# Performance work log

Measured on AMD Instinct MI355X. Metric: run time of the kernel, lower is better.

Reference implementation:

```python
import jax, jax.numpy as jnp
import numpy as np

B, L, D = 4, 896, 2048
HQ, HKV, HD = 32, 8, 64
GROUP = HQ // HKV          # 4
TOKENS_PER_FRAME = 7
ROPE_BASE = 10000.0


def setup_inputs() -> dict:
    key = jax.random.key(0)
    ks = jax.random.split(key, 5)
    s = 0.02
    return {
        "x": jax.random.normal(ks[0], (B, L, D), jnp.float32),
        "wq": jax.random.normal(ks[1], (D, D), jnp.float32) * s,
        "wk": jax.random.normal(ks[2], (D, HKV * HD), jnp.float32) * s,
        "wv": jax.random.normal(ks[3], (D, HKV * HD), jnp.float32) * s,
        "wo": jax.random.normal(ks[4], (D, D), jnp.float32) * s,
        "pos_ids": jnp.arange(L, dtype=jnp.int32),
    }


def _apply_rotary(t, cos, sin):
    # t: [B, L, H, HD]; rotate all HD dims, interleaved pairs.
    Bt, Lt, Ht, Hd = t.shape
    tp = t.reshape(Bt, Lt, Ht, Hd // 2, 2)
    x1, x2 = tp[..., 0], tp[..., 1]
    c = cos[None, :, None, :]   # [1, L, 1, HD/2]
    s = sin[None, :, None, :]
    y1 = x1 * c - x2 * s
    y2 = x1 * s + x2 * c
    return jnp.stack([y1, y2], axis=-1).reshape(Bt, Lt, Ht, Hd)


def reference(x, wq, wk, wv, wo, pos_ids):
    Bx, Lx, Dx = x.shape
    q = (x @ wq).reshape(Bx, Lx, HQ, HD)
    k = (x @ wk).reshape(Bx, Lx, HKV, HD)
    v = (x @ wv).reshape(Bx, Lx, HKV, HD)

    # RoPE (rot_dim = head_dim), scale = 1.0
    half = HD // 2
    inv_freq = 1.0 / (ROPE_BASE ** (jnp.arange(half, dtype=jnp.float32) / half))
    freqs = pos_ids.astype(jnp.float32)[:, None] * inv_freq[None, :]  # [L, HD/2]
    cos, sin = jnp.cos(freqs), jnp.sin(freqs)
    q = _apply_rotary(q, cos, sin)
    k = _apply_rotary(k, cos, sin)

    # GQA: expand kv heads to q heads (kv_head = q_head // GROUP)
    k = jnp.repeat(k, GROUP, axis=2)   # [B, L, HQ, HD]
    v = jnp.repeat(v, GROUP, axis=2)

    scale = 1.0 / jnp.sqrt(jnp.float32(HD))
    scores = jnp.einsum('blhd,bmhd->bhlm', q, k) * scale  # [B, HQ, L, L]

    # frame-block causal mask: allow key frame <= query frame
    pos = jnp.arange(Lx)
    fid = pos // TOKENS_PER_FRAME
    allow = fid[None, :] <= fid[:, None]                  # [L, L]
    neg = jnp.finfo(scores.dtype).min
    scores = jnp.where(allow[None, None], scores, neg)

    probs = jax.nn.softmax(scores, axis=-1)
    out = jnp.einsum('bhlm,bmhd->blhd', probs, v).reshape(Bx, Lx, Dx)
    return out @ wo
```

## Files before the change

### kernel.cpp

```cpp
#include <hip/hip_runtime.h>
#include <hip/hip_bf16.h>
#include <cstdint>

typedef __bf16 bf16;
typedef __bf16 bf16x8 __attribute__((ext_vector_type(8)));
typedef float floatx4 __attribute__((ext_vector_type(4)));

#define B_   4
#define L_   896
#define D_   2048
#define HQ_  32
#define HKV_ 8
#define HD_  64
#define NQKV 3072
#define M_   3584

__device__ inline void gl_lds16(const bf16* g, bf16* l) {
    __builtin_amdgcn_global_load_lds(
        (const __attribute__((address_space(1))) void*)g,
        (__attribute__((address_space(3))) void*)l, 16, 0, 0);
}

__device__ inline void barrier_() {
    asm volatile("" ::: "memory");
    __builtin_amdgcn_s_barrier();
    asm volatile("" ::: "memory");
}

__global__ __launch_bounds__(256) void convert_to_bf16(const float* __restrict__ in,
                                                       bf16* __restrict__ out) {
    long q = (long)blockIdx.x * 256 + threadIdx.x;
    float4 v = ((const float4*)in)[q];
    union { bf16 b[4]; ushort4 u; } w;
    w.b[0] = (bf16)v.x; w.b[1] = (bf16)v.y; w.b[2] = (bf16)v.z; w.b[3] = (bf16)v.w;
    ((ushort4*)out)[q] = w.u;
}

__global__ __launch_bounds__(256) void rope_cs_kernel(const int* __restrict__ pos_ids,
                                                      float2* __restrict__ cs) {
    int idx = blockIdx.x * 256 + threadIdx.x;
    if (idx >= L_ * 32) return;
    int l = idx >> 5, i = idx & 31;
    float p = (float)pos_ids[l];
    float inv = exp2f(-(float)i * (13.287712379549449f / 32.0f));
    float a = p * inv;
    cs[idx] = make_float2(cosf(a), sinf(a));
}

__global__ __launch_bounds__(256) void rope_apply(bf16* __restrict__ QKV,
                                                  const float2* __restrict__ cs) {
    int idx = blockIdx.x * 256 + threadIdx.x;
    int m = idx / 320, g = idx - m * 320;
    int l = m % L_;
    int hp = (g * 4) & 31;
    const float2* ct = &cs[l * 32 + hp];
    bf16* p = QKV + (long)m * NQKV + g * 8;
    bf16x8 v = *(bf16x8*)p;
    bf16x8 w;
#pragma unroll
    for (int i = 0; i < 4; i++) {
        float2 csv = ct[i];
        float x1 = (float)v[2 * i], x2 = (float)v[2 * i + 1];
        w[2 * i]     = (bf16)(x1 * csv.x - x2 * csv.y);
        w[2 * i + 1] = (bf16)(x1 * csv.y + x2 * csv.x);
    }
    *(bf16x8*)p = w;
}

__global__ __launch_bounds__(256) void transpose_cvt(
    const float* __restrict__ in, ushort* __restrict__ out, int C, int R) {
    __shared__ ushort t[64][72];
    int tid = threadIdx.x;
    int tr = tid >> 4, tc = (tid & 15) << 2;
    long r0 = (long)blockIdx.y << 6, c0 = (long)blockIdx.x << 6;
#pragma unroll
    for (int i = 0; i < 4; ++i) {
        float4 v = *(const float4*)&in[(r0 + tr + i * 16) * C + c0 + tc];
        union { bf16 b[4]; ushort4 u; } w;
        w.b[0] = (bf16)v.x; w.b[1] = (bf16)v.y; w.b[2] = (bf16)v.z; w.b[3] = (bf16)v.w;
        *(ushort4*)&t[tr + i * 16][tc] = w.u;
    }
    __syncthreads();
#pragma unroll
    for (int i = 0; i < 4; ++i) {
        ushort4 w;
        w.x = t[tc + 0][tr + i * 16];
        w.y = t[tc + 1][tr + i * 16];
        w.z = t[tc + 2][tr + i * 16];
        w.w = t[tc + 3][tr + i * 16];
        *(ushort4*)&out[(c0 + tr + i * 16) * R + r0 + tc] = w;
    }
}

__global__ __launch_bounds__(256) void transpose_u16(
    const ushort* __restrict__ in, ushort* __restrict__ out,
    int ld_in, int ld_out, long is1, long is2, long os1, long os2) {
    __shared__ ushort t[64][72];
    int z = blockIdx.z;
    const ushort* ip = in + (long)(z >> 3) * is1 + (long)(z & 7) * is2;
    ushort* op = out + (long)(z >> 3) * os1 + (long)(z & 7) * os2;
    int tid = threadIdx.x;
    int tr = tid >> 4, tc = (tid & 15) << 2;
    long r0 = (long)blockIdx.y << 6, c0 = (long)blockIdx.x << 6;
#pragma unroll
    for (int i = 0; i < 4; ++i) {
        ushort4 v = *(const ushort4*)&ip[(r0 + tr + i * 16) * ld_in + c0 + tc];
        *(ushort4*)&t[tr + i * 16][tc] = v;
    }
    __syncthreads();
#pragma unroll
    for (int i = 0; i < 4; ++i) {
        ushort4 w;
        w.x = t[tc + 0][tr + i * 16];
        w.y = t[tc + 1][tr + i * 16];
        w.z = t[tc + 2][tr + i * 16];
        w.w = t[tc + 3][tr + i * 16];
        *(ushort4*)&op[(c0 + tr + i * 16) * ld_out + r0 + tc] = w;
    }
}

template <int JF, int OUTF32>
__global__ __launch_bounds__(512, 2) void gemm224(
    const bf16* __restrict__ A, const bf16* __restrict__ Bt, void* __restrict__ C,
    int Ntot, int Ktot) {
    __shared__ bf16 ldsA[2][224 * 64];
    __shared__ bf16 ldsB[2][JF * 64 * 64];
    const int tid = threadIdx.x;
    const int lane = tid & 63;
    const int quad = lane >> 4, l16 = lane & 15;
    const int w = tid >> 6;
    const int wr = w >> 2, wc = w & 3;

    const int gx = gridDim.x;
    const int nwg = gx * gridDim.y;
    int orig = blockIdx.y * gx + blockIdx.x;
    int q8 = nwg >> 3, r8 = nwg & 7;
    int xcd = orig & 7, lid = orig >> 3;
    int wg = (xcd < r8 ? xcd * (q8 + 1) : r8 * (q8 + 1) + (xcd - r8) * q8) + lid;
    const long m0 = (long)(wg / gx) * 224;
    const long n0 = (long)(wg % gx) * (JF * 64);

    const long rowK = Ktot;
    const int srow = tid >> 3;
    const int scol = ((tid & 7) ^ (srow & 7)) << 3;
    const bf16* baseA = A  + (m0 + srow) * rowK + scol;
    const bf16* baseB = Bt + (n0 + srow) * rowK + scol;
    bf16* const dA = (bf16*)ldsA + tid * 8;
    bf16* const dB = (bf16*)ldsB + tid * 8;

    const int m7 = l16 & 7;
    const int col0 = ((0 + quad) ^ m7) << 3;
    const int col1 = ((4 + quad) ^ m7) << 3;
    const int abase = wr * 112 + l16;
    const int bbase = wc * (JF * 16) + l16;

    floatx4 acc[7][JF];
#pragma unroll
    for (int i = 0; i < 7; ++i)
#pragma unroll
        for (int j = 0; j < JF; ++j)
#pragma unroll
            for (int r = 0; r < 4; ++r) acc[i][j][r] = 0.f;

    bf16x8 af0[4][2], af1[3][2], bq[JF][2];

    const int T = Ktot >> 6;

    {
        gl_lds16(baseA,              dA);
        gl_lds16(baseA + 64 * rowK,  dA + 4096);
        gl_lds16(baseA + 128 * rowK, dA + 8192);
        if (tid < 256) gl_lds16(baseA + 192 * rowK, dA + 12288);
#pragma unroll
        for (int r = 0; r < JF; ++r) gl_lds16(baseB + r * 64 * rowK, dB + r * 4096);
#pragma unroll
        for (int r = 0; r < JF; ++r) gl_lds16(baseB + 64 + r * 64 * rowK,
                                              dB + JF * 4096 + r * 4096);
    }
    if (JF == 3) asm volatile("s_waitcnt vmcnt(3)" ::: "memory");
    else         asm volatile("s_waitcnt vmcnt(2)" ::: "memory");
    barrier_();

    for (int t = 0; t < T; ++t) {
        const int cur = t & 1, nxt = cur ^ 1;
        const bf16* pa = &ldsA[cur][0];
        const bf16* pb = &ldsB[cur][0];
        const long koff  = (long)(t + 1) * 64;
        const long koff2 = (long)(t + 2) * 64;

#pragma unroll
        for (int i = 0; i < 4; ++i) {
            const bf16* rp = &pa[(abase + i * 16) * 64];
            af0[i][0] = *(const bf16x8*)&rp[col0];
            af0[i][1] = *(const bf16x8*)&rp[col1];
        }
#pragma unroll
        for (int j = 0; j < JF; ++j) {
            const bf16* rp = &pb[(bbase + j * 16) * 64];
            bq[j][0] = *(const bf16x8*)&rp[col0];
            bq[j][1] = *(const bf16x8*)&rp[col1];
        }
        if (t + 1 < T) {
            const bf16* g = baseA + koff;
            bf16* l = dA + nxt * (224 * 64);
            gl_lds16(g,              l);
            gl_lds16(g + 64 * rowK,  l + 4096);
            gl_lds16(g + 128 * rowK, l + 8192);
            if (tid < 256) gl_lds16(g + 192 * rowK, l + 12288);
        }
        barrier_();
        asm volatile("s_waitcnt lgkmcnt(0)" ::: "memory");
        __builtin_amdgcn_sched_barrier(0);
        __builtin_amdgcn_s_setprio(1);
#pragma unroll
        for (int i = 0; i < 4; ++i)
#pragma unroll
            for (int j = 0; j < JF; ++j) {
                floatx4 c = acc[i][j];
                c = __builtin_amdgcn_mfma_f32_16x16x32_bf16(af0[i][0], bq[j][0], c, 0, 0, 0);
                c = __builtin_amdgcn_mfma_f32_16x16x32_bf16(af0[i][1], bq[j][1], c, 0, 0, 0);
                acc[i][j] = c;
            }
        __builtin_amdgcn_s_setprio(0);
        barrier_();

#pragma unroll
        for (int i = 0; i < 3; ++i) {
            const bf16* rp = &pa[(abase + (4 + i) * 16) * 64];
            af1[i][0] = *(const bf16x8*)&rp[col0];
            af1[i][1] = *(const bf16x8*)&rp[col1];
        }
        if (t + 2 < T) {
            const bf16* g = baseB + koff2;
            bf16* l = dB + cur * (JF * 64 * 64);
#pragma unroll
            for (int r = 0; r < JF; ++r) gl_lds16(g + r * 64 * rowK, l + r * 4096);
        }
        barrier_();
        asm volatile("s_waitcnt lgkmcnt(0)" ::: "memory");
        __builtin_amdgcn_sched_barrier(0);
        __builtin_amdgcn_s_setprio(1);
#pragma unroll
        for (int i = 0; i < 3; ++i)
#pragma unroll
            for (int j = 0; j < JF; ++j) {
                floatx4 c = acc[4 + i][j];
                c = __builtin_amdgcn_mfma_f32_16x16x32_bf16(af1[i][0], bq[j][0], c, 0, 0, 0);
                c = __builtin_amdgcn_mfma_f32_16x16x32_bf16(af1[i][1], bq[j][1], c, 0, 0, 0);
                acc[4 + i][j] = c;
            }
        __builtin_amdgcn_s_setprio(0);
        if (t + 2 < T) {
            if (JF == 3) asm volatile("s_waitcnt vmcnt(3)" ::: "memory");
            else         asm volatile("s_waitcnt vmcnt(2)" ::: "memory");
        } else {
            asm volatile("s_waitcnt vmcnt(0)" ::: "memory");
        }
        barrier_();
    }

#pragma unroll
    for (int i = 0; i < 7; ++i)
#pragma unroll
        for (int j = 0; j < JF; ++j)
#pragma unroll
            for (int r = 0; r < 4; ++r) {
                long m = m0 + wr * 112 + i * 16 + quad * 4 + r;
                long n = n0 + wc * (JF * 16) + j * 16 + l16;
                if (OUTF32) ((float*)C)[m * Ntot + n] = acc[i][j][r];
                else        ((bf16*)C)[m * Ntot + n] = (bf16)acc[i][j][r];
            }
}

__global__ __launch_bounds__(256) void attn_kernel(
    const bf16* __restrict__ QKV,
    const bf16* __restrict__ Vt,
    bf16* __restrict__ AO) {
    __shared__ bf16 Ks[64 * 64];
    __shared__ bf16 Vs[64 * 64];
    __shared__ bf16 Ps[4][32 * 76];
    const int tid  = threadIdx.x;
    const int wid  = tid >> 6, lane = tid & 63;
    const int quad = lane >> 4, c = lane & 15;
    const int b = blockIdx.z;
    const int kvh = blockIdx.y >> 1, hp = blockIdx.y & 1;
    const int hq = kvh * 4 + hp * 2 + (wid >> 1);
    const int sub = wid & 1;
    const int xpair = blockIdx.x;
    bf16* ps = &Ps[wid][0];

    const bf16* Kb = QKV + ((long)(b * L_)) * NQKV + D_ + kvh * HD_;
    const bf16* Vb = Vt + ((long)(b * HKV_ + kvh)) * (HD_ * L_);

    const int srow = tid >> 3, schunk = (tid & 7) << 3;
    const int sslot = ((tid & 7) ^ (srow & 7)) << 3;
    const bf16* kp0 = &Kb[(long)srow * NQKV + schunk];
    const bf16* kp1 = &Kb[(long)(32 + srow) * NQKV + schunk];
    const bf16* vp0 = &Vb[(long)srow * L_ + schunk];
    const bf16* vp1 = &Vb[(long)(srow + 32) * L_ + schunk];

    const int m7 = c & 7;
    const int col0 = ((0 + quad) ^ m7) << 3;
    const int col1 = ((4 + quad) ^ m7) << 3;

    const floatx4 fzero = {0.f, 0.f, 0.f, 0.f};
    const float C1 = 0.18033688011112042f;

#pragma unroll 1
    for (int pass = 0; pass < 2; ++pass) {
        const int x = pass == 0 ? xpair : 13 - xpair;
        const int q0b = x * 64;
        const bf16* Qb = QKV + ((long)(b * L_ + q0b + sub * 32)) * NQKV + hq * HD_;

        bf16x8 qf[2][2];
#pragma unroll
        for (int a = 0; a < 2; a++) {
            qf[a][0] = *(const bf16x8*)&Qb[(long)(a * 16 + c) * NQKV + quad * 8];
            qf[a][1] = *(const bf16x8*)&Qb[(long)(a * 16 + c) * NQKV + 32 + quad * 8];
        }

        float lsum[2][4];
        floatx4 o[2][4];
#pragma unroll
        for (int a = 0; a < 2; a++)
#pragma unroll
            for (int r = 0; r < 4; r++) lsum[a][r] = 0.f;
#pragma unroll
        for (int a = 0; a < 2; a++)
#pragma unroll
            for (int nt = 0; nt < 4; nt++)
#pragma unroll
                for (int r = 0; r < 4; r++) o[a][nt][r] = 0.f;

        int fe[2][4];
#pragma unroll
        for (int a = 0; a < 2; a++)
#pragma unroll
            for (int r = 0; r < 4; r++) {
                int l = q0b + sub * 32 + a * 16 + quad * 4 + r;
                fe[a][r] = (l / 7 + 1) * 7;
            }
        const int femin = (q0b / 7 + 1) * 7;
        const int kend  = ((q0b + 63) / 7 + 1) * 7;

        bf16x8 kg0 = *(const bf16x8*)&kp0[0];
        bf16x8 kg1 = *(const bf16x8*)&kp1[0];
        bf16x8 vg0 = *(const bf16x8*)&vp0[0];
        bf16x8 vg1 = *(const bf16x8*)&vp1[0];

        for (int k0 = 0; k0 < kend; k0 += 64) {
            __syncthreads();
            *(bf16x8*)&Ks[srow * 64 + sslot]        = kg0;
            *(bf16x8*)&Ks[(srow + 32) * 64 + sslot] = kg1;
            *(bf16x8*)&Vs[srow * 64 + sslot]        = vg0;
            *(bf16x8*)&Vs[(srow + 32) * 64 + sslot] = vg1;
            __syncthreads();

            const int kn = k0 + 64;
            if (kn < kend) {
                kg0 = *(const bf16x8*)&kp0[(long)kn * NQKV];
                kg1 = *(const bf16x8*)&kp1[(long)kn * NQKV];
                vg0 = *(const bf16x8*)&vp0[kn];
                vg1 = *(const bf16x8*)&vp1[kn];
            }

            bf16x8 kf[4][2];
#pragma unroll
            for (int n = 0; n < 4; n++) {
                const bf16* rp = &Ks[(n * 16 + c) * 64];
                kf[n][0] = *(bf16x8*)&rp[col0];
                kf[n][1] = *(bf16x8*)&rp[col1];
            }
            const int masked = (k0 + 64 > femin);
#pragma unroll
            for (int a = 0; a < 2; a++) {
                floatx4 s[4];
#pragma unroll
                for (int n = 0; n < 4; n++) {
                    s[n] = __builtin_amdgcn_mfma_f32_16x16x32_bf16(qf[a][0], kf[n][0], fzero, 0, 0, 0);
                    s[n] = __builtin_amdgcn_mfma_f32_16x16x32_bf16(qf[a][1], kf[n][1], s[n], 0, 0, 0);
                }
                if (masked) {
#pragma unroll
                    for (int n = 0; n < 4; n++) {
                        const int key = k0 + n * 16 + c;
#pragma unroll
                        for (int r = 0; r < 4; r++) {
                            float e = exp2f(s[n][r] * C1);
                            e = (key < fe[a][r]) ? e : 0.f;
                            lsum[a][r] += e;
                            ps[(a * 16 + quad * 4 + r) * 76 + n * 16 + c] = (bf16)e;
                        }
                    }
                } else {
#pragma unroll
                    for (int n = 0; n < 4; n++) {
#pragma unroll
                        for (int r = 0; r < 4; r++) {
                            float e = exp2f(s[n][r] * C1);
                            lsum[a][r] += e;
                            ps[(a * 16 + quad * 4 + r) * 76 + n * 16 + c] = (bf16)e;
                        }
                    }
                }
            }
            bf16x8 vf[4][2];
#pragma unroll
            for (int nt = 0; nt < 4; nt++) {
                const bf16* rp = &Vs[(nt * 16 + c) * 64];
                vf[nt][0] = *(bf16x8*)&rp[col0];
                vf[nt][1] = *(bf16x8*)&rp[col1];
            }
#pragma unroll
            for (int a = 0; a < 2; a++) {
                bf16x8 pf0 = *(bf16x8*)&ps[(a * 16 + c) * 76 + quad * 8];
                bf16x8 pf1 = *(bf16x8*)&ps[(a * 16 + c) * 76 + 32 + quad * 8];
#pragma unroll
                for (int nt = 0; nt < 4; nt++) {
                    o[a][nt] = __builtin_amdgcn_mfma_f32_16x16x32_bf16(pf0, vf[nt][0], o[a][nt], 0, 0, 0);
                    o[a][nt] = __builtin_amdgcn_mfma_f32_16x16x32_bf16(pf1, vf[nt][1], o[a][nt], 0, 0, 0);
                }
            }
        }
#pragma unroll
        for (int a = 0; a < 2; a++)
#pragma unroll
            for (int r = 0; r < 4; r++) {
#pragma unroll
                for (int off = 1; off < 16; off <<= 1)
                    lsum[a][r] += __shfl_xor(lsum[a][r], off);
            }
#pragma unroll
        for (int a = 0; a < 2; a++)
#pragma unroll
            for (int nt = 0; nt < 4; nt++)
#pragma unroll
                for (int r = 0; r < 4; r++) {
                    int l = q0b + sub * 32 + a * 16 + quad * 4 + r;
                    AO[((long)(b * L_ + l)) * D_ + hq * HD_ + nt * 16 + c] =
                        (bf16)(o[a][nt][r] / lsum[a][r]);
                }
    }
}

extern "C" void kernel_launch(void* const* d_in, const int* in_sizes, int n_in,
                              void* d_out, int out_size, void* d_ws, size_t ws_size,
                              hipStream_t stream) {
    (void)in_sizes; (void)n_in; (void)out_size; (void)ws_size;
    const float* x  = (const float*)d_in[0];
    const float* wq = (const float*)d_in[1];
    const float* wk = (const float*)d_in[2];
    const float* wv = (const float*)d_in[3];
    const float* wo = (const float*)d_in[4];
    const int* pos  = (const int*)d_in[5];

    bf16* ws    = (bf16*)d_ws;
    bf16* xb    = ws;
    bf16* wqkvT = ws + 7340032L;
    bf16* woT   = ws + 13631488L;
    bf16* QKV   = ws + 17825792L;
    bf16* Vt    = ws + 28835840L;
    bf16* AO    = xb;
    float2* cs  = (float2*)(ws + 30670848L);

    convert_to_bf16<<<dim3(7168), 256, 0, stream>>>(x, xb);
    rope_cs_kernel<<<dim3(112), dim3(256), 0, stream>>>(pos, cs);

    transpose_cvt<<<dim3(32, 32), 256, 0, stream>>>(wq, (ushort*)wqkvT, 2048, 2048);
    transpose_cvt<<<dim3(8, 32), 256, 0, stream>>>(wk, (ushort*)(wqkvT + 4194304L), 512, 2048);
    transpose_cvt<<<dim3(8, 32), 256, 0, stream>>>(wv, (ushort*)(wqkvT + 5242880L), 512, 2048);
    transpose_cvt<<<dim3(32, 32), 256, 0, stream>>>(wo, (ushort*)woT, 2048, 2048);

    gemm224<3, 0><<<dim3(16, 16), 512, 0, stream>>>(xb, wqkvT, QKV, NQKV, D_);

    rope_apply<<<dim3(4480), 256, 0, stream>>>(QKV, cs);

    transpose_u16<<<dim3(1, 14, 32), 256, 0, stream>>>(
        (const ushort*)(QKV + 2560), (ushort*)Vt, 3072, 896,
        896L * 3072, 64, 8L * 57344, 57344);

    attn_kernel<<<dim3(7, 16, 4), 256, 0, stream>>>(QKV, Vt, AO);

    gemm224<2, 1><<<dim3(16, 16), 512, 0, stream>>>(AO, woT, d_out, D_, D_);
}
```

Baseline: 269.6 us.

## Fuse prep kernels into one launch and double attention KV tile to 128

Merges the x conversion, the four weight transpose-converts and the RoPE cos/sin table into a single prep kernel, so six launches become one and their work shares one grid. The attention kernel now stages 128 keys per iteration, with a wider swizzled V tile, and processes two 64-key halves between barriers. This halves the number of barrier/staging rounds and prefetch phases. The cost is more shared memory and more prefetch registers per block, which may lower occupancy.

```diff
diff --git a/kernel.cpp b/kernel.cpp
--- a/kernel.cpp
+++ b/kernel.cpp
@@ -25,26 +25,6 @@
     asm volatile("" ::: "memory");
     __builtin_amdgcn_s_barrier();
     asm volatile("" ::: "memory");
-}
-
-__global__ __launch_bounds__(256) void convert_to_bf16(const float* __restrict__ in,
-                                                       bf16* __restrict__ out) {
-    long q = (long)blockIdx.x * 256 + threadIdx.x;
-    float4 v = ((const float4*)in)[q];
-    union { bf16 b[4]; ushort4 u; } w;
-    w.b[0] = (bf16)v.x; w.b[1] = (bf16)v.y; w.b[2] = (bf16)v.z; w.b[3] = (bf16)v.w;
-    ((ushort4*)out)[q] = w.u;
-}
-
-__global__ __launch_bounds__(256) void rope_cs_kernel(const int* __restrict__ pos_ids,
-                                                      float2* __restrict__ cs) {
-    int idx = blockIdx.x * 256 + threadIdx.x;
-    if (idx >= L_ * 32) return;
-    int l = idx >> 5, i = idx & 31;
-    float p = (float)pos_ids[l];
-    float inv = exp2f(-(float)i * (13.287712379549449f / 32.0f));
-    float a = p * inv;
-    cs[idx] = make_float2(cosf(a), sinf(a));
 }
 
 __global__ __launch_bounds__(256) void rope_apply(bf16* __restrict__ QKV,
@@ -67,12 +47,11 @@
     *(bf16x8*)p = w;
 }
 
-__global__ __launch_bounds__(256) void transpose_cvt(
-    const float* __restrict__ in, ushort* __restrict__ out, int C, int R) {
-    __shared__ ushort t[64][72];
-    int tid = threadIdx.x;
+__device__ inline void tr_cvt_body(const float* __restrict__ in,
+                                   ushort* __restrict__ out, int C, int R,
+                                   int bx, int by, int tid, ushort (*t)[72]) {
     int tr = tid >> 4, tc = (tid & 15) << 2;
-    long r0 = (long)blockIdx.y << 6, c0 = (long)blockIdx.x << 6;
+    long r0 = (long)by << 6, c0 = (long)bx << 6;
 #pragma unroll
     for (int i = 0; i < 4; ++i) {
         float4 v = *(const float4*)&in[(r0 + tr + i * 16) * C + c0 + tc];
@@ -89,6 +68,44 @@
         w.z = t[tc + 2][tr + i * 16];
         w.w = t[tc + 3][tr + i * 16];
         *(ushort4*)&out[(c0 + tr + i * 16) * R + r0 + tc] = w;
+    }
+}
+
+__global__ __launch_bounds__(256) void prep_kernel(
+    const float* __restrict__ x, const float* __restrict__ wq,
+    const float* __restrict__ wk, const float* __restrict__ wv,
+    const float* __restrict__ wo, const int* __restrict__ pos_ids,
+    bf16* __restrict__ xb, bf16* __restrict__ wqkvT, bf16* __restrict__ woT,
+    float2* __restrict__ cs) {
+    __shared__ ushort t[64][72];
+    const int d = blockIdx.x, tid = threadIdx.x;
+    if (d < 7168) {
+        long q = (long)d * 256 + tid;
+        float4 v = ((const float4*)x)[q];
+        union { bf16 b[4]; ushort4 u; } w;
+        w.b[0] = (bf16)v.x; w.b[1] = (bf16)v.y; w.b[2] = (bf16)v.z; w.b[3] = (bf16)v.w;
+        ((ushort4*)xb)[q] = w.u;
+    } else if (d < 8192) {
+        int e = d - 7168;
+        tr_cvt_body(wq, (ushort*)wqkvT, 2048, 2048, e & 31, e >> 5, tid, t);
+    } else if (d < 9216) {
+        int e = d - 8192;
+        tr_cvt_body(wo, (ushort*)woT, 2048, 2048, e & 31, e >> 5, tid, t);
+    } else if (d < 9472) {
+        int e = d - 9216;
+        tr_cvt_body(wk, (ushort*)(wqkvT + 4194304L), 512, 2048, e & 7, e >> 3, tid, t);
+    } else if (d < 9728) {
+        int e = d - 9472;
+        tr_cvt_body(wv, (ushort*)(wqkvT + 5242880L), 512, 2048, e & 7, e >> 3, tid, t);
+    } else {
+        int idx = (d - 9728) * 256 + tid;
+        if (idx < L_ * 32) {
+            int l = idx >> 5, i = idx & 31;
+            float p = (float)pos_ids[l];
+            float inv = exp2f(-(float)i * (13.287712379549449f / 32.0f));
+            float a = p * inv;
+            cs[idx] = make_float2(cosf(a), sinf(a));
+        }
     }
 }
 
@@ -276,8 +293,8 @@
     const bf16* __restrict__ QKV,
     const bf16* __restrict__ Vt,
     bf16* __restrict__ AO) {
-    __shared__ bf16 Ks[64 * 64];
-    __shared__ bf16 Vs[64 * 64];
+    __shared__ bf16 Ks[128 * 64];
+    __shared__ bf16 Vs[64 * 128];
     __shared__ bf16 Ps[4][32 * 76];
     const int tid  = threadIdx.x;
     const int wid  = tid >> 6, lane = tid & 63;
@@ -292,16 +309,14 @@
     const bf16* Kb = QKV + ((long)(b * L_)) * NQKV + D_ + kvh * HD_;
     const bf16* Vb = Vt + ((long)(b * HKV_ + kvh)) * (HD_ * L_);
 
-    const int srow = tid >> 3, schunk = (tid & 7) << 3;
-    const int sslot = ((tid & 7) ^ (srow & 7)) << 3;
-    const bf16* kp0 = &Kb[(long)srow * NQKV + schunk];
-    const bf16* kp1 = &Kb[(long)(32 + srow) * NQKV + schunk];
-    const bf16* vp0 = &Vb[(long)srow * L_ + schunk];
-    const bf16* vp1 = &Vb[(long)(srow + 32) * L_ + schunk];
+    const int srowK = tid >> 3, schunkK = (tid & 7) << 3;
+    const int sslotK = ((tid & 7) ^ (srowK & 7)) << 3;
+    const int srowV = tid >> 4, schunkV = (tid & 15) << 3;
+    const int sslotV = ((tid & 15) ^ (srowV & 15)) << 3;
 
     const int m7 = c & 7;
-    const int col0 = ((0 + quad) ^ m7) << 3;
-    const int col1 = ((4 + quad) ^ m7) << 3;
+    const int colK0 = ((0 + quad) ^ m7) << 3;
+    const int colK1 = ((4 + quad) ^ m7) << 3;
 
     const floatx4 fzero = {0.f, 0.f, 0.f, 0.f};
     const float C1 = 0.18033688011112042f;
@@ -343,82 +358,95 @@
         const int femin = (q0b / 7 + 1) * 7;
         const int kend  = ((q0b + 63) / 7 + 1) * 7;
 
-        bf16x8 kg0 = *(const bf16x8*)&kp0[0];
-        bf16x8 kg1 = *(const bf16x8*)&kp1[0];
-        bf16x8 vg0 = *(const bf16x8*)&vp0[0];
-        bf16x8 vg1 = *(const bf16x8*)&vp1[0];
-
-        for (int k0 = 0; k0 < kend; k0 += 64) {
+        bf16x8 kgr[4], vgr[4];
+#pragma unroll
+        for (int j = 0; j < 4; j++)
+            kgr[j] = *(const bf16x8*)&Kb[(long)(srowK + 32 * j) * NQKV + schunkK];
+#pragma unroll
+        for (int j = 0; j < 4; j++)
+            vgr[j] = *(const bf16x8*)&Vb[(long)(srowV + 16 * j) * L_ + schunkV];
+
+        for (int k0 = 0; k0 < kend; k0 += 128) {
             __syncthreads();
-            *(bf16x8*)&Ks[srow * 64 + sslot]        = kg0;
-            *(bf16x8*)&Ks[(srow + 32) * 64 + sslot] = kg1;
-            *(bf16x8*)&Vs[srow * 64 + sslot]        = vg0;
-            *(bf16x8*)&Vs[(srow + 32) * 64 + sslot] = vg1;
+#pragma unroll
+            for (int j = 0; j < 4; j++)
+                *(bf16x8*)&Ks[(srowK + 32 * j) * 64 + sslotK] = kgr[j];
+#pragma unroll
+            for (int j = 0; j < 4; j++)
+                *(bf16x8*)&Vs[(srowV + 16 * j) * 128 + sslotV] = vgr[j];
             __syncthreads();
 
-            const int kn = k0 + 64;
+            const int kn = k0 + 128;
             if (kn < kend) {
-                kg0 = *(const bf16x8*)&kp0[(long)kn * NQKV];
-                kg1 = *(const bf16x8*)&kp1[(long)kn * NQKV];
-                vg0 = *(const bf16x8*)&vp0[kn];
-                vg1 = *(const bf16x8*)&vp1[kn];
-            }
-
-            bf16x8 kf[4][2];
-#pragma unroll
-            for (int n = 0; n < 4; n++) {
-                const bf16* rp = &Ks[(n * 16 + c) * 64];
-                kf[n][0] = *(bf16x8*)&rp[col0];
-                kf[n][1] = *(bf16x8*)&rp[col1];
-            }
-            const int masked = (k0 + 64 > femin);
-#pragma unroll
-            for (int a = 0; a < 2; a++) {
-                floatx4 s[4];
+#pragma unroll
+                for (int j = 0; j < 4; j++)
+                    kgr[j] = *(const bf16x8*)&Kb[(long)(kn + srowK + 32 * j) * NQKV + schunkK];
+#pragma unroll
+                for (int j = 0; j < 4; j++)
+                    vgr[j] = *(const bf16x8*)&Vb[(long)(srowV + 16 * j) * L_ + kn + schunkV];
+            }
+
+#pragma unroll
+            for (int h = 0; h < 2; h++) {
+                const int kb = k0 + 64 * h;
+                if (kb >= kend) break;
+
+                bf16x8 kf[4][2];
 #pragma unroll
                 for (int n = 0; n < 4; n++) {
-                    s[n] = __builtin_amdgcn_mfma_f32_16x16x32_bf16(qf[a][0], kf[n][0], fzero, 0, 0, 0);
-                    s[n] = __builtin_amdgcn_mfma_f32_16x16x32_bf16(qf[a][1], kf[n][1], s[n], 0, 0, 0);
+                    const bf16* rp = &Ks[(64 * h + n * 16 + c) * 64];
+                    kf[n][0] = *(bf16x8*)&rp[colK0];
+                    kf[n][1] = *(bf16x8*)&rp[colK1];
                 }
-                if (masked) {
+                const int masked = (kb + 64 > femin);
+#pragma unroll
+                for (int a = 0; a < 2; a++) {
+                    floatx4 s[4];
 #pragma unroll
                     for (int n = 0; n < 4; n++) {
-                        const int key = k0 + n * 16 + c;
-#pragma unroll
-                        for (int r = 0; r < 4; r++) {
-                            float e = exp2f(s[n][r] * C1);
-                            e = (key < fe[a][r]) ? e : 0.f;
-                            lsum[a][r] += e;
-                            ps[(a * 16 + quad * 4 + r) * 76 + n * 16 + c] = (bf16)e;
+                        s[n] = __builtin_amdgcn_mfma_f32_16x16x32_bf16(qf[a][0], kf[n][0], fzero, 0, 0, 0);
+                        s[n] = __builtin_amdgcn_mfma_f32_16x16x32_bf16(qf[a][1], kf[n][1], s[n], 0, 0, 0);
+                    }
+                    if (masked) {
+#pragma unroll
+                        for (int n = 0; n < 4; n++) {
+                            const int key = kb + n * 16 + c;
+#pragma unroll
+                            for (int r = 0; r < 4; r++) {
+                                float e = exp2f(s[n][r] * C1);
+                                e = (key < fe[a][r]) ? e : 0.f;
+                                lsum[a][r] += e;
+                                ps[(a * 16 + quad * 4 + r) * 76 + n * 16 + c] = (bf16)e;
+                            }
                         }
-                    }
-                } else {
-#pragma unroll
-                    for (int n = 0; n < 4; n++) {
-#pragma unroll
-                        for (int r = 0; r < 4; r++) {
-                            float e = exp2f(s[n][r] * C1);
-                            lsum[a][r] += e;
-                            ps[(a * 16 + quad * 4 + r) * 76 + n * 16 + c] = (bf16)e;
+                    } else {
+#pragma unroll
+                        for (int n = 0; n < 4; n++) {
+#pragma unroll
+                            for (int r = 0; r < 4; r++) {
+                                float e = exp2f(s[n][r] * C1);
+                                lsum[a][r] += e;
+                                ps[(a * 16 + quad * 4 + r) * 76 + n * 16 + c] = (bf16)e;
+                            }
                         }
                     }
                 }
-            }
-            bf16x8 vf[4][2];
-#pragma unroll
-            for (int nt = 0; nt < 4; nt++) {
-                const bf16* rp = &Vs[(nt * 16 + c) * 64];
-                vf[nt][0] = *(bf16x8*)&rp[col0];
-                vf[nt][1] = *(bf16x8*)&rp[col1];
-            }
-#pragma unroll
-            for (int a = 0; a < 2; a++) {
-                bf16x8 pf0 = *(bf16x8*)&ps[(a * 16 + c) * 76 + quad * 8];
-                bf16x8 pf1 = *(bf16x8*)&ps[(a * 16 + c) * 76 + 32 + quad * 8];
+                bf16x8 vf[4][2];
 #pragma unroll
                 for (int nt = 0; nt < 4; nt++) {
-                    o[a][nt] = __builtin_amdgcn_mfma_f32_16x16x32_bf16(pf0, vf[nt][0], o[a][nt], 0, 0, 0);
-                    o[a][nt] = __builtin_amdgcn_mfma_f32_16x16x32_bf16(pf1, vf[nt][1], o[a][nt], 0, 0, 0);
+                    const bf16* rp = &Vs[(nt * 16 + c) * 128];
+                    vf[nt][0] = *(bf16x8*)&rp[(((8 * h + 0 + quad) ^ c) << 3)];
+                    vf[nt][1] = *(bf16x8*)&rp[(((8 * h + 4 + quad) ^ c) << 3)];
+                }
+#pragma unroll
+                for (int a = 0; a < 2; a++) {
+                    bf16x8 pf0 = *(bf16x8*)&ps[(a * 16 + c) * 76 + quad * 8];
+                    bf16x8 pf1 = *(bf16x8*)&ps[(a * 16 + c) * 76 + 32 + quad * 8];
+#pragma unroll
+                    for (int nt = 0; nt < 4; nt++) {
+                        o[a][nt] = __builtin_amdgcn_mfma_f32_16x16x32_bf16(pf0, vf[nt][0], o[a][nt], 0, 0, 0);
+                        o[a][nt] = __builtin_amdgcn_mfma_f32_16x16x32_bf16(pf1, vf[nt][1], o[a][nt], 0, 0, 0);
+                    }
                 }
             }
         }
@@ -463,13 +491,8 @@
     bf16* AO    = xb;
     float2* cs  = (float2*)(ws + 30670848L);
 
-    convert_to_bf16<<<dim3(7168), 256, 0, stream>>>(x, xb);
-    rope_cs_kernel<<<dim3(112), dim3(256), 0, stream>>>(pos, cs);
-
-    transpose_cvt<<<dim3(32, 32), 256, 0, stream>>>(wq, (ushort*)wqkvT, 2048, 2048);
-    transpose_cvt<<<dim3(8, 32), 256, 0, stream>>>(wk, (ushort*)(wqkvT + 4194304L), 512, 2048);
-    transpose_cvt<<<dim3(8, 32), 256, 0, stream>>>(wv, (ushort*)(wqkvT + 5242880L), 512, 2048);
-    transpose_cvt<<<dim3(32, 32), 256, 0, stream>>>(wo, (ushort*)woT, 2048, 2048);
+    prep_kernel<<<dim3(9840), 256, 0, stream>>>(x, wq, wk, wv, wo, pos,
+                                                xb, wqkvT, woT, cs);
 
     gemm224<3, 0><<<dim3(16, 16), 512, 0, stream>>>(xb, wqkvT, QKV, NQKV, D_);
 
```

Result: faster. 260.3 us (-3.4%).

## Fuse prep kernels and keep attention P tile in registers via shuffles

Applied to the files above, without the earlier changes.

Six preprocessing launches (x conversion, rope cos/sin table, four weight transpose-converts) are merged into one kernel that dispatches on block index, cutting launch overhead. In attention, S is computed transposed (K as the A operand), so each lane holds scores for one query row. The bf16 probabilities are then repacked into the PV MFMA A-operand layout with lane shuffles instead of a round trip through LDS. This removes the per-wave Ps LDS buffer and its write/read traffic. In exchange it adds many shuffle and select instructions, and the row-sum reduction now uses fewer shuffles.

```diff
diff --git a/kernel.cpp b/kernel.cpp
--- a/kernel.cpp
+++ b/kernel.cpp
@@ -25,26 +25,6 @@
     asm volatile("" ::: "memory");
     __builtin_amdgcn_s_barrier();
     asm volatile("" ::: "memory");
-}
-
-__global__ __launch_bounds__(256) void convert_to_bf16(const float* __restrict__ in,
-                                                       bf16* __restrict__ out) {
-    long q = (long)blockIdx.x * 256 + threadIdx.x;
-    float4 v = ((const float4*)in)[q];
-    union { bf16 b[4]; ushort4 u; } w;
-    w.b[0] = (bf16)v.x; w.b[1] = (bf16)v.y; w.b[2] = (bf16)v.z; w.b[3] = (bf16)v.w;
-    ((ushort4*)out)[q] = w.u;
-}
-
-__global__ __launch_bounds__(256) void rope_cs_kernel(const int* __restrict__ pos_ids,
-                                                      float2* __restrict__ cs) {
-    int idx = blockIdx.x * 256 + threadIdx.x;
-    if (idx >= L_ * 32) return;
-    int l = idx >> 5, i = idx & 31;
-    float p = (float)pos_ids[l];
-    float inv = exp2f(-(float)i * (13.287712379549449f / 32.0f));
-    float a = p * inv;
-    cs[idx] = make_float2(cosf(a), sinf(a));
 }
 
 __global__ __launch_bounds__(256) void rope_apply(bf16* __restrict__ QKV,
@@ -67,12 +47,11 @@
     *(bf16x8*)p = w;
 }
 
-__global__ __launch_bounds__(256) void transpose_cvt(
-    const float* __restrict__ in, ushort* __restrict__ out, int C, int R) {
-    __shared__ ushort t[64][72];
-    int tid = threadIdx.x;
+__device__ inline void tr_cvt_body(const float* __restrict__ in,
+                                   ushort* __restrict__ out, int C, int R,
+                                   int bx, int by, int tid, ushort (*t)[72]) {
     int tr = tid >> 4, tc = (tid & 15) << 2;
-    long r0 = (long)blockIdx.y << 6, c0 = (long)blockIdx.x << 6;
+    long r0 = (long)by << 6, c0 = (long)bx << 6;
 #pragma unroll
     for (int i = 0; i < 4; ++i) {
         float4 v = *(const float4*)&in[(r0 + tr + i * 16) * C + c0 + tc];
@@ -89,6 +68,44 @@
         w.z = t[tc + 2][tr + i * 16];
         w.w = t[tc + 3][tr + i * 16];
         *(ushort4*)&out[(c0 + tr + i * 16) * R + r0 + tc] = w;
+    }
+}
+
+__global__ __launch_bounds__(256) void prep_kernel(
+    const float* __restrict__ x, const float* __restrict__ wq,
+    const float* __restrict__ wk, const float* __restrict__ wv,
+    const float* __restrict__ wo, const int* __restrict__ pos_ids,
+    bf16* __restrict__ xb, bf16* __restrict__ wqkvT, bf16* __restrict__ woT,
+    float2* __restrict__ cs) {
+    __shared__ ushort t[64][72];
+    const int d = blockIdx.x, tid = threadIdx.x;
+    if (d < 7168) {
+        long q = (long)d * 256 + tid;
+        float4 v = ((const float4*)x)[q];
+        union { bf16 b[4]; ushort4 u; } w;
+        w.b[0] = (bf16)v.x; w.b[1] = (bf16)v.y; w.b[2] = (bf16)v.z; w.b[3] = (bf16)v.w;
+        ((ushort4*)xb)[q] = w.u;
+    } else if (d < 8192) {
+        int e = d - 7168;
+        tr_cvt_body(wq, (ushort*)wqkvT, 2048, 2048, e & 31, e >> 5, tid, t);
+    } else if (d < 9216) {
+        int e = d - 8192;
+        tr_cvt_body(wo, (ushort*)woT, 2048, 2048, e & 31, e >> 5, tid, t);
+    } else if (d < 9472) {
+        int e = d - 9216;
+        tr_cvt_body(wk, (ushort*)(wqkvT + 4194304L), 512, 2048, e & 7, e >> 3, tid, t);
+    } else if (d < 9728) {
+        int e = d - 9472;
+        tr_cvt_body(wv, (ushort*)(wqkvT + 5242880L), 512, 2048, e & 7, e >> 3, tid, t);
+    } else {
+        int idx = (d - 9728) * 256 + tid;
+        if (idx < L_ * 32) {
+            int l = idx >> 5, i = idx & 31;
+            float p = (float)pos_ids[l];
+            float inv = exp2f(-(float)i * (13.287712379549449f / 32.0f));
+            float a = p * inv;
+            cs[idx] = make_float2(cosf(a), sinf(a));
+        }
     }
 }
 
@@ -278,16 +295,15 @@
     bf16* __restrict__ AO) {
     __shared__ bf16 Ks[64 * 64];
     __shared__ bf16 Vs[64 * 64];
-    __shared__ bf16 Ps[4][32 * 76];
     const int tid  = threadIdx.x;
-    const int wid  = tid >> 6, lane = tid & 63;
+    const int lane = tid & 63;
+    const int wid  = tid >> 6;
     const int quad = lane >> 4, c = lane & 15;
     const int b = blockIdx.z;
     const int kvh = blockIdx.y >> 1, hp = blockIdx.y & 1;
     const int hq = kvh * 4 + hp * 2 + (wid >> 1);
     const int sub = wid & 1;
     const int xpair = blockIdx.x;
-    bf16* ps = &Ps[wid][0];
 
     const bf16* Kb = QKV + ((long)(b * L_)) * NQKV + D_ + kvh * HD_;
     const bf16* Vb = Vt + ((long)(b * HKV_ + kvh)) * (HD_ * L_);
@@ -303,6 +319,10 @@
     const int col0 = ((0 + quad) ^ m7) << 3;
     const int col1 = ((4 + quad) ^ m7) << 3;
 
+    const int srcA = ((quad & 1) << 5) + c;
+    const int srcB = srcA + 16;
+    const int nsel = quad >> 1;
+
     const floatx4 fzero = {0.f, 0.f, 0.f, 0.f};
     const float C1 = 0.18033688011112042f;
 
@@ -319,27 +339,23 @@
             qf[a][1] = *(const bf16x8*)&Qb[(long)(a * 16 + c) * NQKV + 32 + quad * 8];
         }
 
-        float lsum[2][4];
+        float lsum[2];
         floatx4 o[2][4];
 #pragma unroll
-        for (int a = 0; a < 2; a++)
-#pragma unroll
-            for (int r = 0; r < 4; r++) lsum[a][r] = 0.f;
-#pragma unroll
-        for (int a = 0; a < 2; a++)
+        for (int a = 0; a < 2; a++) {
+            lsum[a] = 0.f;
 #pragma unroll
             for (int nt = 0; nt < 4; nt++)
 #pragma unroll
                 for (int r = 0; r < 4; r++) o[a][nt][r] = 0.f;
-
-        int fe[2][4];
-#pragma unroll
-        for (int a = 0; a < 2; a++)
-#pragma unroll
-            for (int r = 0; r < 4; r++) {
-                int l = q0b + sub * 32 + a * 16 + quad * 4 + r;
-                fe[a][r] = (l / 7 + 1) * 7;
-            }
+        }
+
+        int fe[2];
+#pragma unroll
+        for (int a = 0; a < 2; a++) {
+            int l = q0b + sub * 32 + a * 16 + c;
+            fe[a] = (l / 7 + 1) * 7;
+        }
         const int femin = (q0b / 7 + 1) * 7;
         const int kend  = ((q0b + 63) / 7 + 1) * 7;
 
@@ -371,39 +387,6 @@
                 kf[n][0] = *(bf16x8*)&rp[col0];
                 kf[n][1] = *(bf16x8*)&rp[col1];
             }
-            const int masked = (k0 + 64 > femin);
-#pragma unroll
-            for (int a = 0; a < 2; a++) {
-                floatx4 s[4];
-#pragma unroll
-                for (int n = 0; n < 4; n++) {
-                    s[n] = __builtin_amdgcn_mfma_f32_16x16x32_bf16(qf[a][0], kf[n][0], fzero, 0, 0, 0);
-                    s[n] = __builtin_amdgcn_mfma_f32_16x16x32_bf16(qf[a][1], kf[n][1], s[n], 0, 0, 0);
-                }
-                if (masked) {
-#pragma unroll
-                    for (int n = 0; n < 4; n++) {
-                        const int key = k0 + n * 16 + c;
-#pragma unroll
-                        for (int r = 0; r < 4; r++) {
-                            float e = exp2f(s[n][r] * C1);
-                            e = (key < fe[a][r]) ? e : 0.f;
-                            lsum[a][r] += e;
-                            ps[(a * 16 + quad * 4 + r) * 76 + n * 16 + c] = (bf16)e;
-                        }
-                    }
-                } else {
-#pragma unroll
-                    for (int n = 0; n < 4; n++) {
-#pragma unroll
-                        for (int r = 0; r < 4; r++) {
-                            float e = exp2f(s[n][r] * C1);
-                            lsum[a][r] += e;
-                            ps[(a * 16 + quad * 4 + r) * 76 + n * 16 + c] = (bf16)e;
-                        }
-                    }
-                }
-            }
             bf16x8 vf[4][2];
 #pragma unroll
             for (int nt = 0; nt < 4; nt++) {
@@ -411,35 +394,95 @@
                 vf[nt][0] = *(bf16x8*)&rp[col0];
                 vf[nt][1] = *(bf16x8*)&rp[col1];
             }
+            const int masked = (k0 + 64 > femin);
 #pragma unroll
             for (int a = 0; a < 2; a++) {
-                bf16x8 pf0 = *(bf16x8*)&ps[(a * 16 + c) * 76 + quad * 8];
-                bf16x8 pf1 = *(bf16x8*)&ps[(a * 16 + c) * 76 + 32 + quad * 8];
+                floatx4 s[4];
+#pragma unroll
+                for (int n = 0; n < 4; n++) {
+                    s[n] = __builtin_amdgcn_mfma_f32_16x16x32_bf16(kf[n][0], qf[a][0], fzero, 0, 0, 0);
+                    s[n] = __builtin_amdgcn_mfma_f32_16x16x32_bf16(kf[n][1], qf[a][1], s[n], 0, 0, 0);
+                }
+                float e[4][4];
+                if (masked) {
+#pragma unroll
+                    for (int n = 0; n < 4; n++)
+#pragma unroll
+                        for (int r = 0; r < 4; r++) {
+                            const int key = k0 + n * 16 + quad * 4 + r;
+                            float v = exp2f(s[n][r] * C1);
+                            v = (key < fe[a]) ? v : 0.f;
+                            e[n][r] = v;
+                            lsum[a] += v;
+                        }
+                } else {
+#pragma unroll
+                    for (int n = 0; n < 4; n++)
+#pragma unroll
+                        for (int r = 0; r < 4; r++) {
+                            float v = exp2f(s[n][r] * C1);
+                            e[n][r] = v;
+                            lsum[a] += v;
+                        }
+                }
+                uint pk[4][2];
+#pragma unroll
+                for (int n = 0; n < 4; n++) {
+                    union { bf16 h[2]; uint u; } t0, t1;
+                    t0.h[0] = (bf16)e[n][0]; t0.h[1] = (bf16)e[n][1];
+                    t1.h[0] = (bf16)e[n][2]; t1.h[1] = (bf16)e[n][3];
+                    pk[n][0] = t0.u; pk[n][1] = t1.u;
+                }
+                union { uint u[4]; bf16x8 v; } pf0, pf1;
+                {
+                    uint a0 = __shfl((int)pk[0][0], srcA);
+                    uint a1 = __shfl((int)pk[1][0], srcA);
+                    pf0.u[0] = nsel ? a1 : a0;
+                    uint b0 = __shfl((int)pk[0][1], srcA);
+                    uint b1 = __shfl((int)pk[1][1], srcA);
+                    pf0.u[1] = nsel ? b1 : b0;
+                    uint c0_ = __shfl((int)pk[0][0], srcB);
+                    uint c1_ = __shfl((int)pk[1][0], srcB);
+                    pf0.u[2] = nsel ? c1_ : c0_;
+                    uint d0 = __shfl((int)pk[0][1], srcB);
+                    uint d1 = __shfl((int)pk[1][1], srcB);
+                    pf0.u[3] = nsel ? d1 : d0;
+                    uint e0 = __shfl((int)pk[2][0], srcA);
+                    uint e1 = __shfl((int)pk[3][0], srcA);
+                    pf1.u[0] = nsel ? e1 : e0;
+                    uint f0 = __shfl((int)pk[2][1], srcA);
+                    uint f1 = __shfl((int)pk[3][1], srcA);
+                    pf1.u[1] = nsel ? f1 : f0;
+                    uint g0 = __shfl((int)pk[2][0], srcB);
+                    uint g1 = __shfl((int)pk[3][0], srcB);
+                    pf1.u[2] = nsel ? g1 : g0;
+                    uint h0 = __shfl((int)pk[2][1], srcB);
+                    uint h1 = __shfl((int)pk[3][1], srcB);
+                    pf1.u[3] = nsel ? h1 : h0;
+                }
 #pragma unroll
                 for (int nt = 0; nt < 4; nt++) {
-                    o[a][nt] = __builtin_amdgcn_mfma_f32_16x16x32_bf16(pf0, vf[nt][0], o[a][nt], 0, 0, 0);
-                    o[a][nt] = __builtin_amdgcn_mfma_f32_16x16x32_bf16(pf1, vf[nt][1], o[a][nt], 0, 0, 0);
+                    o[a][nt] = __builtin_amdgcn_mfma_f32_16x16x32_bf16(pf0.v, vf[nt][0], o[a][nt], 0, 0, 0);
+                    o[a][nt] = __builtin_amdgcn_mfma_f32_16x16x32_bf16(pf1.v, vf[nt][1], o[a][nt], 0, 0, 0);
                 }
             }
         }
 #pragma unroll
+        for (int a = 0; a < 2; a++) {
+            lsum[a] += __shfl_xor(lsum[a], 16);
+            lsum[a] += __shfl_xor(lsum[a], 32);
+        }
+#pragma unroll
         for (int a = 0; a < 2; a++)
 #pragma unroll
             for (int r = 0; r < 4; r++) {
-#pragma unroll
-                for (int off = 1; off < 16; off <<= 1)
-                    lsum[a][r] += __shfl_xor(lsum[a][r], off);
-            }
-#pragma unroll
-        for (int a = 0; a < 2; a++)
-#pragma unroll
-            for (int nt = 0; nt < 4; nt++)
-#pragma unroll
-                for (int r = 0; r < 4; r++) {
-                    int l = q0b + sub * 32 + a * 16 + quad * 4 + r;
+                float ls = __shfl(lsum[a], (lane & 48) + quad * 4 + r);
+                int l = q0b + sub * 32 + a * 16 + quad * 4 + r;
+#pragma unroll
+                for (int nt = 0; nt < 4; nt++)
                     AO[((long)(b * L_ + l)) * D_ + hq * HD_ + nt * 16 + c] =
-                        (bf16)(o[a][nt][r] / lsum[a][r]);
-                }
+                        (bf16)(o[a][nt][r] / ls);
+            }
     }
 }
 
@@ -463,13 +506,8 @@
     bf16* AO    = xb;
     float2* cs  = (float2*)(ws + 30670848L);
 
-    convert_to_bf16<<<dim3(7168), 256, 0, stream>>>(x, xb);
-    rope_cs_kernel<<<dim3(112), dim3(256), 0, stream>>>(pos, cs);
-
-    transpose_cvt<<<dim3(32, 32), 256, 0, stream>>>(wq, (ushort*)wqkvT, 2048, 2048);
-    transpose_cvt<<<dim3(8, 32), 256, 0, stream>>>(wk, (ushort*)(wqkvT + 4194304L), 512, 2048);
-    transpose_cvt<<<dim3(8, 32), 256, 0, stream>>>(wv, (ushort*)(wqkvT + 5242880L), 512, 2048);
-    transpose_cvt<<<dim3(32, 32), 256, 0, stream>>>(wo, (ushort*)woT, 2048, 2048);
+    prep_kernel<<<dim3(9840), 256, 0, stream>>>(x, wq, wk, wv, wo, pos,
+                                                xb, wqkvT, woT, cs);
 
     gemm224<3, 0><<<dim3(16, 16), 512, 0, stream>>>(xb, wqkvT, QKV, NQKV, D_);
 
```

Measured after the change: 251.3 us. 6.8% less time.
